# Kernel optimization log

Measured on AMD Instinct MI355X. Metric: run time of the kernel, lower is better.

The kernel has to match this reference:

```python
import jax, jax.numpy as jnp
import numpy as np

MARGIN = 0.3
EPS = 1e-6  # torch TripletMarginLoss pairwise_distance eps


def setup_inputs() -> dict:
    key = jax.random.key(0)
    k1, k2 = jax.random.split(key)
    n, d = 8192, 128
    inputs = jax.random.normal(k1, (n, d), dtype=jnp.float32)
    similarity = jax.random.randint(k2, (n, n), 0, 2, dtype=jnp.int32)
    return {"inputs": inputs, "similarity": similarity}


def reference(inputs, similarity):
    # mask[i, j] = True if j is a positive of anchor i
    mask = similarity != 0                      # (n, n) bool
    maskf = mask.astype(inputs.dtype)
    counts = maskf.sum(axis=1, keepdims=True)   # (n, 1), >0 by construction
    # per-anchor center = mean of its positives (masked mean as a GEMM)
    centers = (maskf @ inputs) / counts         # (n, d)
    # dist[i, j] = ||centers[i] - inputs[j]||_2 via the expansion trick
    # (avoids materializing the (n, n, d) difference tensor of the original)
    c2 = jnp.sum(centers * centers, axis=1)[:, None]
    x2 = jnp.sum(inputs * inputs, axis=1)[None, :]
    d2 = c2 + x2 - 2.0 * (centers @ inputs.T)
    dist = jnp.sqrt(jnp.maximum(d2, 0.0))       # (n, n)
    # dist only feeds argmin in the original (indices carry no grad)
    dist = jax.lax.stop_gradient(dist)
    # hard-negative mining: argmin of dist over negatives of each anchor
    neg_idx = jnp.argmin(jnp.where(mask, jnp.inf, dist), axis=1)  # (n,)
    neg_min = inputs[neg_idx]                   # (n, d)
    # TripletMarginLoss(margin=0.3, p=2): anchor=centers, pos=inputs, neg=neg_min
    d_ap = jnp.linalg.norm(centers - inputs + EPS, axis=1)
    d_an = jnp.linalg.norm(centers - neg_min + EPS, axis=1)
    return jnp.mean(jnp.maximum(d_ap - d_an + MARGIN, 0.0))
```

## Files before the change

kernel.cpp:

```cpp
#include <hip/hip_runtime.h>
#include <stdint.h>

#define NN 8192
#define DD 128

typedef float f32x4 __attribute__((ext_vector_type(4)));
typedef short bf16x8 __attribute__((ext_vector_type(8)));

union B8 { uint32_t u[4]; bf16x8 v; };

__device__ inline uint16_t f2bf(float f) {
  uint32_t u = __builtin_bit_cast(uint32_t, f);
  uint32_t r = (u + 0x7FFFu + ((u >> 16) & 1u)) >> 16;
  return (uint16_t)r;
}

__device__ inline f32x4 mfma16(bf16x8 a, bf16x8 b, f32x4 c) {
  return __builtin_amdgcn_mfma_f32_16x16x32_bf16(a, b, c, 0, 0, 0);
}

__global__ __launch_bounds__(256) void k_prep(const float* __restrict__ inp,
                                              uint16_t* __restrict__ inp_bf,
                                              uint16_t* __restrict__ inpT_bf,
                                              float* __restrict__ x2p,
                                              uint32_t* __restrict__ counts,
                                              uint32_t* __restrict__ negkey,
                                              float* __restrict__ out) {
  __shared__ uint16_t ldsT[128 * 65];
  __shared__ float ldsS[256];
  const int tid = threadIdx.x;
  const int gid = blockIdx.x * 256 + tid;
  if (gid < NN) { counts[gid] = 0u; negkey[gid] = 0xFFFFFFFFu; }
  if (gid == 0) out[0] = 0.f;
  const int j0 = blockIdx.x * 64;
  const int r = tid >> 2;
  const int dseg = (tid & 3) * 32;
  float ss = 0.f;
#pragma unroll
  for (int it = 0; it < 8; ++it) {
    float4 v = *(const float4*)(inp + (size_t)(j0 + r) * DD + dseg + it * 4);
    ss += v.x * v.x + v.y * v.y + v.z * v.z + v.w * v.w;
    uint16_t b0 = f2bf(v.x), b1 = f2bf(v.y), b2 = f2bf(v.z), b3 = f2bf(v.w);
    *(ushort4*)(inp_bf + (size_t)(j0 + r) * DD + dseg + it * 4) = make_ushort4(b0, b1, b2, b3);
    int d = dseg + it * 4;
    ldsT[(d + 0) * 65 + r] = b0;
    ldsT[(d + 1) * 65 + r] = b1;
    ldsT[(d + 2) * 65 + r] = b2;
    ldsT[(d + 3) * 65 + r] = b3;
  }
  ldsS[tid] = ss;
  __syncthreads();
  if (tid < 64)
    x2p[j0 + tid] = ldsS[tid * 4] + ldsS[tid * 4 + 1] + ldsS[tid * 4 + 2] + ldsS[tid * 4 + 3] + 512.0f;
#pragma unroll
  for (int it = 0; it < 32; ++it) {
    int flat = it * 256 + tid;
    int d = flat >> 6, jl = flat & 63;
    inpT_bf[(size_t)d * NN + j0 + jl] = ldsT[d * 65 + jl];
  }
}

__global__ __launch_bounds__(256, 2) void k_bitgen(const int* __restrict__ sim,
                                                   uint32_t* __restrict__ bmT,
                                                   uint32_t* __restrict__ counts) {
  __shared__ uint32_t ldsW[64 * 64];
  const int tid = threadIdx.x, lane = tid & 63, w = tid >> 6;
  const int m0 = blockIdx.x * 64;
  const int c0 = blockIdx.y * 2048;
  int va[32], vb[32];
  {
    const int* p = sim + (size_t)(m0 + w) * NN + c0 + lane;
#pragma unroll
    for (int s = 0; s < 32; ++s) va[s] = p[s * 64];
  }
#pragma unroll 1
  for (int rr = 0; rr < 16; ++rr) {
    const int rl = rr * 4 + w;
    if (rr < 15) {
      const int* p = sim + (size_t)(m0 + rl + 4) * NN + c0 + lane;
#pragma unroll
      for (int s = 0; s < 32; ++s) vb[s] = p[s * 64];
    }
    uint32_t cnt = 0;
#pragma unroll
    for (int s = 0; s < 32; ++s) {
      unsigned long long ball = __ballot(va[s] != 0);
      cnt += (uint32_t)__popcll(ball);
      if ((lane & 31) == 0)
        ldsW[(s * 2 + (lane >> 5)) * 64 + rl] = (uint32_t)(ball >> (lane & 32));
    }
    if (lane == 0) atomicAdd(&counts[m0 + rl], cnt);
#pragma unroll
    for (int s = 0; s < 32; ++s) va[s] = vb[s];
  }
  __syncthreads();
#pragma unroll
  for (int it = 0; it < 16; ++it) {
    int idx = it * 256 + tid;
    int kw = idx >> 6, r = idx & 63;
    bmT[(size_t)((c0 >> 5) + kw) * NN + m0 + r] = ldsW[idx];
  }
}

__global__ __launch_bounds__(256, 2) void k_gemm1(const uint16_t* __restrict__ inpT,
                                                  const uint32_t* __restrict__ bmT,
                                                  float* __restrict__ part) {
  const int tid = threadIdx.x, lane = tid & 63, w = tid >> 6;
  const int col = lane & 15, quad = lane >> 4;
  const int m0 = blockIdx.x * 128;
  const int kb0 = blockIdx.y * 1024;
  const int wm = (w >> 1) * 64, wn = (w & 1) * 64;
  f32x4 acc[4][4];
  const f32x4 z = {0.f, 0.f, 0.f, 0.f};
#pragma unroll
  for (int r = 0; r < 4; ++r)
#pragma unroll
    for (int c = 0; c < 4; ++c) acc[r][c] = z;

  bf16x8 bpA[8], bpB[8];
  uint32_t mwA[8], mwB[8];

#define LOADK(BP, MW, KB)                                                                     \
  {                                                                                           \
    _Pragma("unroll") for (int cc = 0; cc < 4; ++cc)                                          \
      _Pragma("unroll") for (int h = 0; h < 2; ++h)                                           \
        BP[cc * 2 + h] =                                                                      \
            *(const bf16x8*)(inpT + (size_t)(wn + cc * 16 + col) * NN + (KB) + h * 32 + quad * 8); \
    _Pragma("unroll") for (int rr = 0; rr < 4; ++rr)                                          \
      _Pragma("unroll") for (int h = 0; h < 2; ++h)                                           \
        MW[rr * 2 + h] = bmT[(size_t)(((KB) >> 5) + h) * NN + m0 + wm + rr * 16 + col];       \
  }

#define STEPK(BP, MW)                                                                         \
  {                                                                                           \
    _Pragma("unroll") for (int h = 0; h < 2; ++h) {                                           \
      B8 af[4];                                                                               \
      _Pragma("unroll") for (int rr = 0; rr < 4; ++rr) {                                      \
        uint32_t word = MW[rr * 2 + h];                                                       \
        uint32_t b = (word >> (quad * 8)) & 0xFFu;                                            \
        uint32_t s = b * 0x8001u;                                                             \
        _Pragma("unroll") for (int p = 0; p < 4; ++p)                                         \
          af[rr].u[p] = ((s >> (2 * p)) & 0x10001u) * 0x3F80u;                                \
      }                                                                                       \
      _Pragma("unroll") for (int cc = 0; cc < 4; ++cc) {                                      \
        bf16x8 bfr = BP[cc * 2 + h];                                                          \
        _Pragma("unroll") for (int rr = 0; rr < 4; ++rr)                                      \
          acc[rr][cc] = mfma16(af[rr].v, bfr, acc[rr][cc]);                                   \
      }                                                                                       \
    }                                                                                         \
  }

  LOADK(bpA, mwA, kb0);
#pragma unroll 1
  for (int ks = 0; ks < 16; ks += 2) {
    const int kb = kb0 + ks * 64;
    LOADK(bpB, mwB, kb + 64);
    STEPK(bpA, mwA);
    if (ks + 2 < 16) LOADK(bpA, mwA, kb + 128);
    STEPK(bpB, mwB);
  }
#undef LOADK
#undef STEPK

  float* pp = part + (size_t)blockIdx.y * NN * DD;
#pragma unroll
  for (int rr = 0; rr < 4; ++rr)
#pragma unroll
    for (int cc = 0; cc < 4; ++cc)
#pragma unroll
      for (int g = 0; g < 4; ++g)
        pp[(size_t)(m0 + wm + rr * 16 + quad * 4 + g) * DD + wn + cc * 16 + col] = acc[rr][cc][g];
}

__global__ __launch_bounds__(256) void k_reduce(const float* __restrict__ part,
                                                const uint32_t* __restrict__ counts,
                                                float* __restrict__ centers,
                                                uint16_t* __restrict__ cen_bf) {
  const int gid = blockIdx.x * 256 + threadIdx.x;
  const int idx = gid * 4;
  const int row = idx >> 7;
  const float inv = 1.0f / (float)counts[row];
  float4 v = *(const float4*)(part + idx);
#pragma unroll
  for (int s = 1; s < 8; ++s) {
    float4 u = *(const float4*)(part + (size_t)s * NN * DD + idx);
    v.x += u.x; v.y += u.y; v.z += u.z; v.w += u.w;
  }
  v.x *= inv; v.y *= inv; v.z *= inv; v.w *= inv;
  *(float4*)(centers + idx) = v;
  *(ushort4*)(cen_bf + idx) = make_ushort4(f2bf(v.x), f2bf(v.y), f2bf(v.z), f2bf(v.w));
}

__global__ __launch_bounds__(256, 2) void k_argmin(const uint16_t* __restrict__ cen_bf,
                                                   const uint16_t* __restrict__ inp_bf,
                                                   const uint32_t* __restrict__ bmT,
                                                   const float* __restrict__ x2p,
                                                   uint32_t* __restrict__ negkey) {
  const int tid = threadIdx.x, lane = tid & 63, w = tid >> 6;
  const int col = lane & 15, quad = lane >> 4;
  const int i0 = blockIdx.x * 128;
  const int jbase = blockIdx.y * 1024;
  const int wi = w * 32;

  bf16x8 af[2][4];
#pragma unroll
  for (int rr = 0; rr < 2; ++rr)
#pragma unroll
    for (int kk = 0; kk < 4; ++kk)
      af[rr][kk] = *(const bf16x8*)(cen_bf + (size_t)(i0 + wi + rr * 16 + col) * DD + kk * 32 + quad * 8);

  uint32_t best[2][4];
#pragma unroll
  for (int rr = 0; rr < 2; ++rr)
#pragma unroll
    for (int g = 0; g < 4; ++g) best[rr][g] = 0xFFFFFFFFu;

  const f32x4 z = {0.f, 0.f, 0.f, 0.f};
  bf16x8 bpA[8], bpB[8];
  uint32_t mwA[8], mwB[8];
  float xvA[2], xvB[2];

#define LOADJ(BP, MW, XV, J0)                                                                 \
  {                                                                                           \
    _Pragma("unroll") for (int cc = 0; cc < 2; ++cc)                                          \
      _Pragma("unroll") for (int kk = 0; kk < 4; ++kk)                                        \
        BP[cc * 4 + kk] =                                                                     \
            *(const bf16x8*)(inp_bf + (size_t)((J0) + cc * 16 + col) * DD + kk * 32 + quad * 8); \
    _Pragma("unroll") for (int rr = 0; rr < 2; ++rr)                                          \
      _Pragma("unroll") for (int g = 0; g < 4; ++g)                                           \
        MW[rr * 4 + g] = bmT[(size_t)((J0) >> 5) * NN + i0 + wi + rr * 16 + quad * 4 + g];    \
    _Pragma("unroll") for (int cc = 0; cc < 2; ++cc) XV[cc] = x2p[(J0) + cc * 16 + col];      \
  }

#define STEPJ(BP, MW, XV, J0)                                                                 \
  {                                                                                           \
    f32x4 acc[2][2];                                                                          \
    acc[0][0] = z; acc[0][1] = z; acc[1][0] = z; acc[1][1] = z;                               \
    _Pragma("unroll") for (int kk = 0; kk < 4; ++kk) {                                        \
      bf16x8 b0 = BP[kk];                                                                     \
      bf16x8 b1 = BP[4 + kk];                                                                 \
      acc[0][0] = mfma16(af[0][kk], b0, acc[0][0]);                                           \
      acc[0][1] = mfma16(af[0][kk], b1, acc[0][1]);                                           \
      acc[1][0] = mfma16(af[1][kk], b0, acc[1][0]);                                           \
      acc[1][1] = mfma16(af[1][kk], b1, acc[1][1]);                                           \
    }                                                                                         \
    _Pragma("unroll") for (int cc = 0; cc < 2; ++cc) {                                        \
      const float xq = XV[cc];                                                                \
      const uint32_t jpre = (uint32_t)((J0) + cc * 16 + col);                                 \
      const int sh = 31 - (cc * 16 + col);                                                    \
      _Pragma("unroll") for (int rr = 0; rr < 2; ++rr)                                        \
        _Pragma("unroll") for (int g = 0; g < 4; ++g) {                                       \
          float v = fmaf(-2.0f, acc[rr][cc][g], xq);                                          \
          uint32_t u = __builtin_bit_cast(uint32_t, v);                                       \
          uint32_t key = (u & 0xFFFFE000u) | jpre;                                            \
          key |= (MW[rr * 4 + g] << sh) & 0x80000000u;                                        \
          best[rr][g] = min(best[rr][g], key);                                                \
        }                                                                                     \
    }                                                                                         \
  }

  LOADJ(bpA, mwA, xvA, jbase);
#pragma unroll 1
  for (int st = 0; st < 32; st += 2) {
    const int j0 = jbase + st * 32;
    LOADJ(bpB, mwB, xvB, j0 + 32);
    STEPJ(bpA, mwA, xvA, j0);
    if (st + 2 < 32) LOADJ(bpA, mwA, xvA, j0 + 64);
    STEPJ(bpB, mwB, xvB, j0 + 32);
  }
#undef LOADJ
#undef STEPJ

#pragma unroll
  for (int rr = 0; rr < 2; ++rr)
#pragma unroll
    for (int g = 0; g < 4; ++g) {
      uint32_t k = best[rr][g];
#pragma unroll
      for (int d = 1; d < 16; d <<= 1) {
        uint32_t o = (uint32_t)__shfl_xor((int)k, d);
        k = min(k, o);
      }
      if (col == 0) atomicMin(&negkey[i0 + wi + rr * 16 + quad * 4 + g], k);
    }
}

__global__ __launch_bounds__(256) void k_loss(const float* __restrict__ centers,
                                              const float* __restrict__ inp,
                                              const uint32_t* __restrict__ negkey,
                                              float* __restrict__ out) {
  __shared__ float lds[4];
  const int tid = threadIdx.x, lane = tid & 63, w = tid >> 6;
  float local = 0.f;
#pragma unroll 1
  for (int a = 0; a < 4; ++a) {
    int i = blockIdx.x * 16 + w * 4 + a;
    float2 c = *(const float2*)(centers + (size_t)i * DD + lane * 2);
    float2 x = *(const float2*)(inp + (size_t)i * DD + lane * 2);
    uint32_t ni = negkey[i] & (NN - 1);
    float2 gv = *(const float2*)(inp + (size_t)ni * DD + lane * 2);
    float e0 = c.x - x.x + 1e-6f, e1 = c.y - x.y + 1e-6f;
    float f0 = c.x - gv.x + 1e-6f, f1 = c.y - gv.y + 1e-6f;
    float dap = e0 * e0 + e1 * e1;
    float dan = f0 * f0 + f1 * f1;
#pragma unroll
    for (int d = 32; d; d >>= 1) {
      dap += __shfl_down(dap, d);
      dan += __shfl_down(dan, d);
    }
    if (lane == 0) local += fmaxf(sqrtf(dap) - sqrtf(dan) + 0.3f, 0.f);
  }
  if (lane == 0) lds[w] = local;
  __syncthreads();
  if (tid == 0) atomicAdd(out, (lds[0] + lds[1] + lds[2] + lds[3]) * (1.0f / 8192.0f));
}

extern "C" void kernel_launch(void* const* d_in, const int* in_sizes, int n_in,
                              void* d_out, int out_size, void* d_ws, size_t ws_size,
                              hipStream_t stream) {
  (void)in_sizes; (void)n_in; (void)out_size; (void)ws_size;
  const float* inp = (const float*)d_in[0];
  const int* sim = (const int*)d_in[1];
  float* out = (float*)d_out;
  char* ws = (char*)d_ws;

  uint32_t* bmT     = (uint32_t*)ws;
  float* part       = (float*)(ws + (8u << 20));
  float* centers    = (float*)(ws + (40u << 20));
  uint16_t* inp_bf  = (uint16_t*)(ws + (44u << 20));
  uint16_t* inpT_bf = (uint16_t*)(ws + (46u << 20));
  uint16_t* cen_bf  = (uint16_t*)(ws + (48u << 20));
  float* x2p        = (float*)(ws + (50u << 20));
  uint32_t* counts  = (uint32_t*)(ws + (50u << 20) + 32768u);
  uint32_t* negkey  = (uint32_t*)(ws + (50u << 20) + 65536u);

  k_prep<<<128, 256, 0, stream>>>(inp, inp_bf, inpT_bf, x2p, counts, negkey, out);
  k_bitgen<<<dim3(128, 4), 256, 0, stream>>>(sim, bmT, counts);
  k_gemm1<<<dim3(64, 8), 256, 0, stream>>>(inpT_bf, bmT, part);
  k_reduce<<<1024, 256, 0, stream>>>(part, counts, centers, cen_bf);
  k_argmin<<<dim3(64, 8), 256, 0, stream>>>(cen_bf, inp_bf, bmT, x2p, negkey);
  k_loss<<<512, 256, 0, stream>>>(centers, inp, negkey, out);
}
```

Measured before the change: 490.1 us.

## Stage GEMM B operands through swizzled LDS via direct global-to-LDS loads

Both the centers GEMM and the argmin distance GEMM now stage their B operands (inpT tiles and inp_bf rows) into double-buffered, XOR-swizzled shared memory using global_load_lds, instead of each wave loading its own fragments from global memory into registers. The argmin kernel also widens each step from 32 to 64 columns per wave. The aim is to share B tiles across waves, cutting redundant global traffic and register pressure, with bank-conflict-free LDS reads. In exchange it adds block-wide barriers and LDS usage that could limit occupancy.

```diff
diff --git a/kernel.cpp b/kernel.cpp
--- a/kernel.cpp
+++ b/kernel.cpp
@@ -17,6 +17,11 @@
 
 __device__ inline f32x4 mfma16(bf16x8 a, bf16x8 b, f32x4 c) {
   return __builtin_amdgcn_mfma_f32_16x16x32_bf16(a, b, c, 0, 0, 0);
+}
+
+__device__ inline void gl_lds16(const uint16_t* g, uint16_t* l) {
+  __builtin_amdgcn_global_load_lds((const __attribute__((address_space(1))) void*)g,
+                                   (__attribute__((address_space(3))) void*)l, 16, 0, 0);
 }
 
 __global__ __launch_bounds__(256) void k_prep(const float* __restrict__ inp,
@@ -105,11 +110,13 @@
 __global__ __launch_bounds__(256, 2) void k_gemm1(const uint16_t* __restrict__ inpT,
                                                   const uint32_t* __restrict__ bmT,
                                                   float* __restrict__ part) {
+  __shared__ __align__(16) uint16_t ldsB[2][128 * 64];
   const int tid = threadIdx.x, lane = tid & 63, w = tid >> 6;
   const int col = lane & 15, quad = lane >> 4;
   const int m0 = blockIdx.x * 128;
   const int kb0 = blockIdx.y * 1024;
   const int wm = (w >> 1) * 64, wn = (w & 1) * 64;
+  const int swz = (col & 7) << 4;
   f32x4 acc[4][4];
   const f32x4 z = {0.f, 0.f, 0.f, 0.f};
 #pragma unroll
@@ -117,21 +124,27 @@
 #pragma unroll
     for (int c = 0; c < 4; ++c) acc[r][c] = z;
 
-  bf16x8 bpA[8], bpB[8];
   uint32_t mwA[8], mwB[8];
-
-#define LOADK(BP, MW, KB)                                                                     \
-  {                                                                                           \
-    _Pragma("unroll") for (int cc = 0; cc < 4; ++cc)                                          \
-      _Pragma("unroll") for (int h = 0; h < 2; ++h)                                           \
-        BP[cc * 2 + h] =                                                                      \
-            *(const bf16x8*)(inpT + (size_t)(wn + cc * 16 + col) * NN + (KB) + h * 32 + quad * 8); \
+  const int srow = lane >> 3;
+  const int schk = (lane & 7) ^ (srow & 7);
+
+#define STAGE3(BUF, KB)                                                                       \
+  {                                                                                           \
+    _Pragma("unroll") for (int c = 0; c < 4; ++c) {                                           \
+      const uint16_t* gsrc =                                                                  \
+          inpT + (size_t)(w * 32 + c * 8 + srow) * NN + (KB) + (schk << 3);                   \
+      gl_lds16(gsrc, &ldsB[BUF][(w * 32 + c * 8) * 64]);                                      \
+    }                                                                                         \
+  }
+
+#define LDM3(MW, KB)                                                                          \
+  {                                                                                           \
     _Pragma("unroll") for (int rr = 0; rr < 4; ++rr)                                          \
       _Pragma("unroll") for (int h = 0; h < 2; ++h)                                           \
         MW[rr * 2 + h] = bmT[(size_t)(((KB) >> 5) + h) * NN + m0 + wm + rr * 16 + col];       \
   }
 
-#define STEPK(BP, MW)                                                                         \
+#define COMP3(BUF, MW)                                                                        \
   {                                                                                           \
     _Pragma("unroll") for (int h = 0; h < 2; ++h) {                                           \
       B8 af[4];                                                                               \
@@ -142,25 +155,35 @@
         _Pragma("unroll") for (int p = 0; p < 4; ++p)                                         \
           af[rr].u[p] = ((s >> (2 * p)) & 0x10001u) * 0x3F80u;                                \
       }                                                                                       \
+      const int eoff = ((h * 64 + quad * 16) ^ swz) >> 1;                                     \
       _Pragma("unroll") for (int cc = 0; cc < 4; ++cc) {                                      \
-        bf16x8 bfr = BP[cc * 2 + h];                                                          \
+        bf16x8 bfr = *(const bf16x8*)(&ldsB[BUF][(wn + cc * 16 + col) * 64 + eoff]);          \
         _Pragma("unroll") for (int rr = 0; rr < 4; ++rr)                                      \
           acc[rr][cc] = mfma16(af[rr].v, bfr, acc[rr][cc]);                                   \
       }                                                                                       \
     }                                                                                         \
   }
 
-  LOADK(bpA, mwA, kb0);
+  STAGE3(0, kb0);
+  LDM3(mwA, kb0);
+  __syncthreads();
 #pragma unroll 1
   for (int ks = 0; ks < 16; ks += 2) {
     const int kb = kb0 + ks * 64;
-    LOADK(bpB, mwB, kb + 64);
-    STEPK(bpA, mwA);
-    if (ks + 2 < 16) LOADK(bpA, mwA, kb + 128);
-    STEPK(bpB, mwB);
-  }
-#undef LOADK
-#undef STEPK
+    STAGE3(1, kb + 64);
+    LDM3(mwB, kb + 64);
+    COMP3(0, mwA);
+    __syncthreads();
+    if (ks + 2 < 16) {
+      STAGE3(0, kb + 128);
+      LDM3(mwA, kb + 128);
+    }
+    COMP3(1, mwB);
+    __syncthreads();
+  }
+#undef STAGE3
+#undef LDM3
+#undef COMP3
 
   float* pp = part + (size_t)blockIdx.y * NN * DD;
 #pragma unroll
@@ -196,11 +219,13 @@
                                                    const uint32_t* __restrict__ bmT,
                                                    const float* __restrict__ x2p,
                                                    uint32_t* __restrict__ negkey) {
+  __shared__ __align__(16) uint16_t ldsX[2][64 * 128];
   const int tid = threadIdx.x, lane = tid & 63, w = tid >> 6;
   const int col = lane & 15, quad = lane >> 4;
   const int i0 = blockIdx.x * 128;
   const int jbase = blockIdx.y * 1024;
   const int wi = w * 32;
+  const int swz = (col & 7) << 4;
 
   bf16x8 af[2][4];
 #pragma unroll
@@ -216,60 +241,69 @@
     for (int g = 0; g < 4; ++g) best[rr][g] = 0xFFFFFFFFu;
 
   const f32x4 z = {0.f, 0.f, 0.f, 0.f};
-  bf16x8 bpA[8], bpB[8];
-  uint32_t mwA[8], mwB[8];
-  float xvA[2], xvB[2];
-
-#define LOADJ(BP, MW, XV, J0)                                                                 \
-  {                                                                                           \
-    _Pragma("unroll") for (int cc = 0; cc < 2; ++cc)                                          \
-      _Pragma("unroll") for (int kk = 0; kk < 4; ++kk)                                        \
-        BP[cc * 4 + kk] =                                                                     \
-            *(const bf16x8*)(inp_bf + (size_t)((J0) + cc * 16 + col) * DD + kk * 32 + quad * 8); \
+  const int srow = lane >> 4;
+
+#define STAGE5(BUF, J0)                                                                       \
+  {                                                                                           \
+    _Pragma("unroll") for (int c = 0; c < 4; ++c) {                                           \
+      const int r7 = (c * 4 + srow) & 7;                                                      \
+      const uint16_t* gsrc =                                                                  \
+          inp_bf + (size_t)((J0) + w * 16 + c * 4 + srow) * DD + (((lane & 15) ^ r7) << 3);   \
+      gl_lds16(gsrc, &ldsX[BUF][(w * 16 + c * 4) * 128]);                                     \
+    }                                                                                         \
+  }
+
+#define COMP5(BUF, J0)                                                                        \
+  {                                                                                           \
+    uint32_t mw[2][2][4];                                                                     \
+    float xv[4];                                                                              \
+    _Pragma("unroll") for (int h = 0; h < 2; ++h)                                             \
+      _Pragma("unroll") for (int rr = 0; rr < 2; ++rr)                                        \
+        _Pragma("unroll") for (int g = 0; g < 4; ++g)                                         \
+          mw[h][rr][g] =                                                                      \
+              bmT[(size_t)(((J0) >> 5) + h) * NN + i0 + wi + rr * 16 + quad * 4 + g];         \
+    _Pragma("unroll") for (int cc = 0; cc < 4; ++cc) xv[cc] = x2p[(J0) + cc * 16 + col];      \
+    f32x4 acc[2][4];                                                                          \
     _Pragma("unroll") for (int rr = 0; rr < 2; ++rr)                                          \
-      _Pragma("unroll") for (int g = 0; g < 4; ++g)                                           \
-        MW[rr * 4 + g] = bmT[(size_t)((J0) >> 5) * NN + i0 + wi + rr * 16 + quad * 4 + g];    \
-    _Pragma("unroll") for (int cc = 0; cc < 2; ++cc) XV[cc] = x2p[(J0) + cc * 16 + col];      \
-  }
-
-#define STEPJ(BP, MW, XV, J0)                                                                 \
-  {                                                                                           \
-    f32x4 acc[2][2];                                                                          \
-    acc[0][0] = z; acc[0][1] = z; acc[1][0] = z; acc[1][1] = z;                               \
+      _Pragma("unroll") for (int cc = 0; cc < 4; ++cc) acc[rr][cc] = z;                       \
     _Pragma("unroll") for (int kk = 0; kk < 4; ++kk) {                                        \
-      bf16x8 b0 = BP[kk];                                                                     \
-      bf16x8 b1 = BP[4 + kk];                                                                 \
-      acc[0][0] = mfma16(af[0][kk], b0, acc[0][0]);                                           \
-      acc[0][1] = mfma16(af[0][kk], b1, acc[0][1]);                                           \
-      acc[1][0] = mfma16(af[1][kk], b0, acc[1][0]);                                           \
-      acc[1][1] = mfma16(af[1][kk], b1, acc[1][1]);                                           \
-    }                                                                                         \
-    _Pragma("unroll") for (int cc = 0; cc < 2; ++cc) {                                        \
-      const float xq = XV[cc];                                                                \
-      const uint32_t jpre = (uint32_t)((J0) + cc * 16 + col);                                 \
-      const int sh = 31 - (cc * 16 + col);                                                    \
+      const int eoff = ((kk * 64 + quad * 16) ^ swz) >> 1;                                    \
+      _Pragma("unroll") for (int cc = 0; cc < 4; ++cc) {                                      \
+        bf16x8 b = *(const bf16x8*)(&ldsX[BUF][(cc * 16 + col) * 128 + eoff]);                \
+        acc[0][cc] = mfma16(af[0][kk], b, acc[0][cc]);                                        \
+        acc[1][cc] = mfma16(af[1][kk], b, acc[1][cc]);                                        \
+      }                                                                                       \
+    }                                                                                         \
+    _Pragma("unroll") for (int cc = 0; cc < 4; ++cc) {                                        \
+      const int jj = cc * 16 + col;                                                           \
+      const float xq = xv[cc];                                                                \
+      const uint32_t jpre = (uint32_t)((J0) + jj);                                            \
+      const int sh = 31 - ((cc & 1) * 16 + col);                                              \
       _Pragma("unroll") for (int rr = 0; rr < 2; ++rr)                                        \
         _Pragma("unroll") for (int g = 0; g < 4; ++g) {                                       \
           float v = fmaf(-2.0f, acc[rr][cc][g], xq);                                          \
           uint32_t u = __builtin_bit_cast(uint32_t, v);                                       \
           uint32_t key = (u & 0xFFFFE000u) | jpre;                                            \
-          key |= (MW[rr * 4 + g] << sh) & 0x80000000u;                                        \
+          key |= (mw[cc >> 1][rr][g] << sh) & 0x80000000u;                                    \
           best[rr][g] = min(best[rr][g], key);                                                \
         }                                                                                     \
     }                                                                                         \
   }
 
-  LOADJ(bpA, mwA, xvA, jbase);
+  STAGE5(0, jbase);
+  __syncthreads();
 #pragma unroll 1
-  for (int st = 0; st < 32; st += 2) {
-    const int j0 = jbase + st * 32;
-    LOADJ(bpB, mwB, xvB, j0 + 32);
-    STEPJ(bpA, mwA, xvA, j0);
-    if (st + 2 < 32) LOADJ(bpA, mwA, xvA, j0 + 64);
-    STEPJ(bpB, mwB, xvB, j0 + 32);
-  }
-#undef LOADJ
-#undef STEPJ
+  for (int st = 0; st < 16; st += 2) {
+    const int j0 = jbase + st * 64;
+    STAGE5(1, j0 + 64);
+    COMP5(0, j0);
+    __syncthreads();
+    if (st + 2 < 16) STAGE5(0, j0 + 128);
+    COMP5(1, j0 + 64);
+    __syncthreads();
+  }
+#undef STAGE5
+#undef COMP5
 
 #pragma unroll
   for (int rr = 0; rr < 2; ++rr)
```

Measured after the change: 443.2 us. -9.6%, faster.
